# Kernel tuning notes

Measured on AMD Instinct MI355X. Metric: run time of the kernel, lower is better.

## Reference

```python
import jax, jax.numpy as jnp
import numpy as np

N_NODES = 50000
N_EDGES = 800000
IN_FEATS = 128
HIDDEN = 128
DNN_H = 256
N_CLASSES = 40


def setup_inputs() -> dict:
    key = jax.random.key(0)
    ks = jax.random.split(key, 12)
    features = jax.random.normal(ks[0], (N_NODES, IN_FEATS), dtype=jnp.float32)
    src = jax.random.randint(ks[1], (N_EDGES,), 0, N_NODES, dtype=jnp.int32)
    dst = jax.random.randint(ks[2], (N_EDGES,), 0, N_NODES, dtype=jnp.int32)
    def lin(k, fi, fo):
        s = 1.0 / np.sqrt(fi)
        return jax.random.uniform(k, (fi, fo), jnp.float32, -s, s)
    W1 = lin(ks[3], IN_FEATS, HIDDEN)
    b1 = jnp.zeros((HIDDEN,), jnp.float32)
    W2 = lin(ks[4], HIDDEN, HIDDEN)
    b2 = jnp.zeros((HIDDEN,), jnp.float32)
    Wd1 = lin(ks[5], HIDDEN, DNN_H)
    bd1 = jnp.zeros((DNN_H,), jnp.float32)
    Wd2 = lin(ks[6], DNN_H, N_CLASSES)
    bd2 = jnp.zeros((N_CLASSES,), jnp.float32)
    return {"features": features, "src": src, "dst": dst,
            "W1": W1, "b1": b1, "W2": W2, "b2": b2,
            "Wd1": Wd1, "bd1": bd1, "Wd2": Wd2, "bd2": bd2}


def _graph_conv(x, src, dst, W, b):
    # dgl GraphConv, norm='both': D_out^{-1/2} -> sum-aggregate -> D_in^{-1/2} -> linear -> relu
    ones = jnp.ones((src.shape[0],), x.dtype)
    deg_out = jax.ops.segment_sum(ones, src, num_segments=N_NODES)
    deg_in = jax.ops.segment_sum(ones, dst, num_segments=N_NODES)
    inv_sqrt_out = jax.lax.rsqrt(jnp.maximum(deg_out, 1.0))  # clamp zero-degree to 1 like dgl
    inv_sqrt_in = jax.lax.rsqrt(jnp.maximum(deg_in, 1.0))
    x = x * inv_sqrt_out[:, None]
    h = jax.ops.segment_sum(x[src], dst, num_segments=N_NODES)  # [N, d] sparse SpMM
    h = h * inv_sqrt_in[:, None]
    return jax.nn.relu(h @ W + b)


def reference(features, src, dst, W1, b1, W2, b2, Wd1, bd1, Wd2, bd2):
    h = _graph_conv(features, src, dst, W1, b1)   # dropout = identity (eval)
    h = _graph_conv(h, src, dst, W2, b2)
    # DNN: Linear -> LeakyReLU(0.01) -> (dropout identity), x2
    h = jax.nn.leaky_relu(h @ Wd1 + bd1, negative_slope=0.01)
    h = jax.nn.leaky_relu(h @ Wd2 + bd2, negative_slope=0.01)
    return h
```

## Files before the change

### kernel.cpp

```cpp
#include <hip/hip_runtime.h>


#define SCAN_B 256

typedef __attribute__((ext_vector_type(8))) short short8v;
typedef __attribute__((ext_vector_type(4))) float f32x4;

__global__ void k_degree_rank(const int* __restrict__ src, const int* __restrict__ dst,
                              int* __restrict__ deg_out, int* __restrict__ deg_in,
                              int* __restrict__ rank, int E) {
    int i = blockIdx.x * blockDim.x + threadIdx.x;
    if (i < E) {
        atomicAdd(&deg_out[src[i]], 1);
        rank[i] = atomicAdd(&deg_in[dst[i]], 1);
    }
}

__global__ void k_scanA(const int* __restrict__ deg_in, int* __restrict__ incl,
                        int* __restrict__ bsum, int N) {
    __shared__ int s[SCAN_B];
    int t = threadIdx.x, i = blockIdx.x * SCAN_B + t;
    int v = (i < N) ? deg_in[i] : 0;
    s[t] = v; __syncthreads();
    for (int o = 1; o < SCAN_B; o <<= 1) {
        int x = (t >= o) ? s[t - o] : 0;
        __syncthreads();
        s[t] += x;
        __syncthreads();
    }
    if (i < N) incl[i] = s[t];
    if (t == SCAN_B - 1) bsum[blockIdx.x] = s[t];
}

__global__ void k_scanB(int* __restrict__ bsum, int NB) {
    __shared__ int s[SCAN_B];
    int t = threadIdx.x;
    int v = (t < NB) ? bsum[t] : 0;
    s[t] = v; __syncthreads();
    for (int o = 1; o < SCAN_B; o <<= 1) {
        int x = (t >= o) ? s[t - o] : 0;
        __syncthreads();
        s[t] += x;
        __syncthreads();
    }
    if (t < NB) bsum[t] = s[t] - v;
}

__global__ void k_scanC(const int* __restrict__ deg_in, const int* __restrict__ deg_out,
                        int* __restrict__ row_ptr, const int* __restrict__ bsum,
                        float* __restrict__ inv_in, float* __restrict__ inv_out,
                        int N, int E) {
    int t = threadIdx.x, i = blockIdx.x * SCAN_B + t;
    if (i < N) {
        int di = deg_in[i];
        row_ptr[i] = row_ptr[i] - di + bsum[blockIdx.x];
        inv_in[i]  = rsqrtf(fmaxf((float)di, 1.0f));
        inv_out[i] = rsqrtf(fmaxf((float)deg_out[i], 1.0f));
    }
    if (i == 0) row_ptr[N] = E;
}

__global__ void k_scatter2(const int* __restrict__ src, const int* __restrict__ dst,
                           const int* __restrict__ row_ptr, const int* __restrict__ rank,
                           int* __restrict__ edge_src, int E) {
    int i = blockIdx.x * blockDim.x + threadIdx.x;
    if (i < E) {
        edge_src[row_ptr[dst[i]] + rank[i]] = src[i];
    }
}

__global__ void k_gather(const float* __restrict__ X, const int* __restrict__ edge_src,
                         const int* __restrict__ row_ptr, const float* __restrict__ inv_out,
                         const float* __restrict__ inv_in, float* __restrict__ Y, int N) {
    int lane = threadIdx.x & 31;
    int row = blockIdx.x * 8 + (threadIdx.x >> 5);
    if (row >= N) return;
    int rs = row_ptr[row], re = row_ptr[row + 1];
    float4 acc = {0.f, 0.f, 0.f, 0.f};
    for (int e = rs; e < re; ++e) {
        int s = edge_src[e];
        float sc = inv_out[s];
        float4 xv = *reinterpret_cast<const float4*>(&X[(size_t)s * 128 + lane * 4]);
        acc.x += xv.x * sc; acc.y += xv.y * sc; acc.z += xv.z * sc; acc.w += xv.w * sc;
    }
    float si = inv_in[row];
    float4 o = {acc.x * si, acc.y * si, acc.z * si, acc.w * si};
    *reinterpret_cast<float4*>(&Y[(size_t)row * 128 + lane * 4]) = o;
}

__device__ inline unsigned short bf16_rne(float f) {
    unsigned int u = __float_as_uint(f);
    u += 0x7fffu + ((u >> 16) & 1u);
    return (unsigned short)(u >> 16);
}

__device__ inline void split1(float a, unsigned short& h, unsigned short& l) {
    unsigned short hh = bf16_rne(a);
    float hf = __uint_as_float((unsigned int)hh << 16);
    l = bf16_rne(a - hf);
    h = hh;
}

template<int K, int N, int ACT>
__global__ __launch_bounds__(256) void k_gemm_mfma(const float* __restrict__ A,
                                                   const float* __restrict__ W,
                                                   const float* __restrict__ bias,
                                                   float* __restrict__ C, int M) {
    __shared__ unsigned short Bh[64 * K], Bl[64 * K];
    __shared__ unsigned short Ah[128 * 32], Al[128 * 32];

    int t = threadIdx.x;
    int m0 = blockIdx.x * 128;
    int cb = blockIdx.y * 64;

    {
        int c = t & 63;
        int kb = (t >> 6) * (K / 4);
        bool cok = (N % 64 == 0) || (cb + c < N);
        for (int j = 0; j < K / 4; ++j) {
            int k = kb + j;
            float v = cok ? W[(size_t)k * N + cb + c] : 0.f;
            unsigned short hi, lo; split1(v, hi, lo);
            int byte = (c * 2 * K + 2 * k) ^ ((c & 7) << 4);
            Bh[byte >> 1] = hi;
            Bl[byte >> 1] = lo;
        }
    }

    f32x4 acc[4][2];
    #pragma unroll
    for (int i = 0; i < 4; ++i)
        #pragma unroll
        for (int j = 0; j < 2; ++j)
            acc[i][j] = (f32x4){0.f, 0.f, 0.f, 0.f};

    int lane = t & 63;
    int wave = t >> 6;
    int wm = wave >> 1, wn = wave & 1;
    int lr = lane & 15, lg = lane >> 4;

    for (int kt = 0; kt < K / 32; ++kt) {
        __syncthreads();
        #pragma unroll
        for (int i = 0; i < 4; ++i) {
            int g = i * 256 + t;
            int r = g >> 3;
            int kq = (g & 7) * 4;
            int gr = m0 + r;
            float4 v = {0.f, 0.f, 0.f, 0.f};
            if (gr < M) v = *reinterpret_cast<const float4*>(&A[(size_t)gr * K + kt * 32 + kq]);
            ushort4 h4, l4;
            split1(v.x, h4.x, l4.x);
            split1(v.y, h4.y, l4.y);
            split1(v.z, h4.z, l4.z);
            split1(v.w, h4.w, l4.w);
            int byte = (r * 64 + 2 * kq) ^ ((r & 7) << 4);
            *reinterpret_cast<ushort4*>(&Ah[byte >> 1]) = h4;
            *reinterpret_cast<ushort4*>(&Al[byte >> 1]) = l4;
        }
        __syncthreads();

        short8v bhf[2], blf[2];
        #pragma unroll
        for (int nf = 0; nf < 2; ++nf) {
            int c = wn * 32 + nf * 16 + lr;
            int byte = (c * 2 * K + 2 * (kt * 32 + lg * 8)) ^ ((c & 7) << 4);
            bhf[nf] = *reinterpret_cast<const short8v*>(&Bh[byte >> 1]);
            blf[nf] = *reinterpret_cast<const short8v*>(&Bl[byte >> 1]);
        }
        #pragma unroll
        for (int mf = 0; mf < 4; ++mf) {
            int r = wm * 64 + mf * 16 + lr;
            int byte = (r * 64 + 2 * (lg * 8)) ^ ((r & 7) << 4);
            short8v ahf = *reinterpret_cast<const short8v*>(&Ah[byte >> 1]);
            short8v alf = *reinterpret_cast<const short8v*>(&Al[byte >> 1]);
            #pragma unroll
            for (int nf = 0; nf < 2; ++nf) {
                acc[mf][nf] = __builtin_amdgcn_mfma_f32_16x16x32_bf16(ahf, bhf[nf], acc[mf][nf], 0, 0, 0);
                acc[mf][nf] = __builtin_amdgcn_mfma_f32_16x16x32_bf16(ahf, blf[nf], acc[mf][nf], 0, 0, 0);
                acc[mf][nf] = __builtin_amdgcn_mfma_f32_16x16x32_bf16(alf, bhf[nf], acc[mf][nf], 0, 0, 0);
            }
        }
    }

    #pragma unroll
    for (int mf = 0; mf < 4; ++mf) {
        #pragma unroll
        for (int nf = 0; nf < 2; ++nf) {
            int col = cb + wn * 32 + nf * 16 + lr;
            if ((N % 64 != 0) && col >= N) continue;
            float bv = bias[col];
            #pragma unroll
            for (int rg = 0; rg < 4; ++rg) {
                int row = m0 + wm * 64 + mf * 16 + lg * 4 + rg;
                if (row < M) {
                    float v = acc[mf][nf][rg] + bv;
                    if (ACT == 0) v = fmaxf(v, 0.f);
                    else v = (v > 0.f) ? v : 0.01f * v;
                    C[(size_t)row * N + col] = v;
                }
            }
        }
    }
}

extern "C" void kernel_launch(void* const* d_in, const int* in_sizes, int n_in,
                              void* d_out, int out_size, void* d_ws, size_t ws_size,
                              hipStream_t stream) {
    const float* feat = (const float*)d_in[0];
    const int*   src  = (const int*)d_in[1];
    const int*   dst  = (const int*)d_in[2];
    const float* W1   = (const float*)d_in[3];
    const float* b1   = (const float*)d_in[4];
    const float* W2   = (const float*)d_in[5];
    const float* b2   = (const float*)d_in[6];
    const float* Wd1  = (const float*)d_in[7];
    const float* bd1  = (const float*)d_in[8];
    const float* Wd2  = (const float*)d_in[9];
    const float* bd2  = (const float*)d_in[10];
    float* out = (float*)d_out;

    const int N = in_sizes[0] / 128;
    const int E = in_sizes[1];

    char* ws = (char*)d_ws;
    size_t off = 0;
    auto alloc = [&](size_t bytes) -> void* {
        void* p = ws + off;
        off += (bytes + 255) & ~(size_t)255;
        return p;
    };
    int* deg_out  = (int*)alloc((size_t)N * 4);
    int* deg_in   = (int*)alloc((size_t)N * 4);
    int* row_ptr  = (int*)alloc((size_t)(N + 1) * 4);
    int* bsum     = (int*)alloc(SCAN_B * 4);
    int* rank     = (int*)alloc((size_t)E * 4);
    int* edge_src = (int*)alloc((size_t)E * 4);
    float* inv_out = (float*)alloc((size_t)N * 4);
    float* inv_in  = (float*)alloc((size_t)N * 4);
    float* agg = (float*)alloc((size_t)N * 128 * 4);
    float* h   = (float*)alloc((size_t)N * 128 * 4);
    float* hd  = (float*)alloc((size_t)N * 256 * 4);

    size_t zspan = (char*)deg_in + (size_t)N * 4 - (char*)deg_out;
    hipMemsetAsync(deg_out, 0, zspan, stream);

    int gE = (E + 255) / 256;
    int gN = (N + SCAN_B - 1) / SCAN_B;
    k_degree_rank<<<gE, 256, 0, stream>>>(src, dst, deg_out, deg_in, rank, E);
    k_scanA<<<gN, SCAN_B, 0, stream>>>(deg_in, row_ptr, bsum, N);
    k_scanB<<<1, SCAN_B, 0, stream>>>(bsum, gN);
    k_scanC<<<gN, SCAN_B, 0, stream>>>(deg_in, deg_out, row_ptr, bsum, inv_in, inv_out, N, E);
    k_scatter2<<<gE, 256, 0, stream>>>(src, dst, row_ptr, rank, edge_src, E);

    int gG = (N + 7) / 8;
    int gMM = (N + 127) / 128;

    k_gather<<<gG, 256, 0, stream>>>(feat, edge_src, row_ptr, inv_out, inv_in, agg, N);
    k_gemm_mfma<128, 128, 0><<<dim3(gMM, 2), 256, 0, stream>>>(agg, W1, b1, h, N);
    k_gather<<<gG, 256, 0, stream>>>(h, edge_src, row_ptr, inv_out, inv_in, agg, N);
    k_gemm_mfma<128, 128, 0><<<dim3(gMM, 2), 256, 0, stream>>>(agg, W2, b2, h, N);
    k_gemm_mfma<128, 256, 1><<<dim3(gMM, 4), 256, 0, stream>>>(h, Wd1, bd1, hd, N);
    k_gemm_mfma<256, 40, 1><<<dim3(gMM, 1), 256, 0, stream>>>(hd, Wd2, bd2, out, N);
}
```

Measured before the change: 379.1 us.

## Fuse degree counting into first GEMM, reorder GEMM before aggregation, pack edge weights

The first graph-conv layer now runs its linear transform before aggregation, which is valid because aggregation is linear. Bias and ReLU move into the gather kernel's epilogue. The degree/rank atomics are folded into the first GEMM launch, which removes a separate kernel. The scatter writes (src, inv_out[src]) pairs so the gather avoids a dependent lookup per edge, and the gather loop is unrolled by four to keep more row loads in flight. The cost is twice the memory for the edge array, and atomics contending inside GEMM blocks.

```diff
diff --git a/kernel.cpp b/kernel.cpp
--- a/kernel.cpp
+++ b/kernel.cpp
@@ -5,16 +5,6 @@
 
 typedef __attribute__((ext_vector_type(8))) short short8v;
 typedef __attribute__((ext_vector_type(4))) float f32x4;
-
-__global__ void k_degree_rank(const int* __restrict__ src, const int* __restrict__ dst,
-                              int* __restrict__ deg_out, int* __restrict__ deg_in,
-                              int* __restrict__ rank, int E) {
-    int i = blockIdx.x * blockDim.x + threadIdx.x;
-    if (i < E) {
-        atomicAdd(&deg_out[src[i]], 1);
-        rank[i] = atomicAdd(&deg_in[dst[i]], 1);
-    }
-}
 
 __global__ void k_scanA(const int* __restrict__ deg_in, int* __restrict__ incl,
                         int* __restrict__ bsum, int N) {
@@ -60,31 +50,54 @@
     if (i == 0) row_ptr[N] = E;
 }
 
-__global__ void k_scatter2(const int* __restrict__ src, const int* __restrict__ dst,
+__global__ void k_scatter3(const int* __restrict__ src, const int* __restrict__ dst,
                            const int* __restrict__ row_ptr, const int* __restrict__ rank,
-                           int* __restrict__ edge_src, int E) {
+                           const float* __restrict__ inv_out,
+                           int2* __restrict__ edges, int E) {
     int i = blockIdx.x * blockDim.x + threadIdx.x;
     if (i < E) {
-        edge_src[row_ptr[dst[i]] + rank[i]] = src[i];
-    }
-}
-
-__global__ void k_gather(const float* __restrict__ X, const int* __restrict__ edge_src,
-                         const int* __restrict__ row_ptr, const float* __restrict__ inv_out,
-                         const float* __restrict__ inv_in, float* __restrict__ Y, int N) {
+        int s = src[i];
+        int2 p;
+        p.x = s;
+        p.y = __float_as_int(inv_out[s]);
+        edges[row_ptr[dst[i]] + rank[i]] = p;
+    }
+}
+
+__global__ void k_gather2(const float* __restrict__ X, const int2* __restrict__ edges,
+                          const int* __restrict__ row_ptr, const float* __restrict__ inv_in,
+                          const float* __restrict__ bias, float* __restrict__ Y, int N) {
     int lane = threadIdx.x & 31;
     int row = blockIdx.x * 8 + (threadIdx.x >> 5);
     if (row >= N) return;
     int rs = row_ptr[row], re = row_ptr[row + 1];
     float4 acc = {0.f, 0.f, 0.f, 0.f};
-    for (int e = rs; e < re; ++e) {
-        int s = edge_src[e];
-        float sc = inv_out[s];
-        float4 xv = *reinterpret_cast<const float4*>(&X[(size_t)s * 128 + lane * 4]);
-        acc.x += xv.x * sc; acc.y += xv.y * sc; acc.z += xv.z * sc; acc.w += xv.w * sc;
-    }
+    int e = rs;
+    #define LDROW(s) (*reinterpret_cast<const float4*>(&X[(size_t)(s) * 128 + lane * 4]))
+    for (; e + 4 <= re; e += 4) {
+        int2 p0 = edges[e], p1 = edges[e + 1], p2 = edges[e + 2], p3 = edges[e + 3];
+        float4 x0 = LDROW(p0.x), x1 = LDROW(p1.x), x2 = LDROW(p2.x), x3 = LDROW(p3.x);
+        float c0 = __int_as_float(p0.y), c1 = __int_as_float(p1.y);
+        float c2 = __int_as_float(p2.y), c3 = __int_as_float(p3.y);
+        acc.x += c0 * x0.x + c1 * x1.x + c2 * x2.x + c3 * x3.x;
+        acc.y += c0 * x0.y + c1 * x1.y + c2 * x2.y + c3 * x3.y;
+        acc.z += c0 * x0.z + c1 * x1.z + c2 * x2.z + c3 * x3.z;
+        acc.w += c0 * x0.w + c1 * x1.w + c2 * x2.w + c3 * x3.w;
+    }
+    for (; e < re; ++e) {
+        int2 p = edges[e];
+        float c = __int_as_float(p.y);
+        float4 xv = LDROW(p.x);
+        acc.x += c * xv.x; acc.y += c * xv.y; acc.z += c * xv.z; acc.w += c * xv.w;
+    }
+    #undef LDROW
     float si = inv_in[row];
-    float4 o = {acc.x * si, acc.y * si, acc.z * si, acc.w * si};
+    float4 b4 = *reinterpret_cast<const float4*>(&bias[lane * 4]);
+    float4 o;
+    o.x = fmaxf(fmaf(acc.x, si, b4.x), 0.f);
+    o.y = fmaxf(fmaf(acc.y, si, b4.y), 0.f);
+    o.z = fmaxf(fmaf(acc.z, si, b4.z), 0.f);
+    o.w = fmaxf(fmaf(acc.w, si, b4.w), 0.f);
     *reinterpret_cast<float4*>(&Y[(size_t)row * 128 + lane * 4]) = o;
 }
 
@@ -101,15 +114,31 @@
     h = hh;
 }
 
-template<int K, int N, int ACT>
+template<int K, int N, int ACT, bool DEG>
 __global__ __launch_bounds__(256) void k_gemm_mfma(const float* __restrict__ A,
                                                    const float* __restrict__ W,
                                                    const float* __restrict__ bias,
-                                                   float* __restrict__ C, int M) {
+                                                   float* __restrict__ C, int M,
+                                                   const int* __restrict__ src,
+                                                   const int* __restrict__ dst,
+                                                   int* __restrict__ deg_out,
+                                                   int* __restrict__ deg_in,
+                                                   int* __restrict__ rank, int E, int epb) {
     __shared__ unsigned short Bh[64 * K], Bl[64 * K];
     __shared__ unsigned short Ah[128 * 32], Al[128 * 32];
 
     int t = threadIdx.x;
+
+    if (DEG) {
+        int bid = blockIdx.y * gridDim.x + blockIdx.x;
+        int base = bid * epb;
+        int end = min(E, base + epb);
+        for (int i = base + t; i < end; i += 256) {
+            atomicAdd(&deg_out[src[i]], 1);
+            rank[i] = atomicAdd(&deg_in[dst[i]], 1);
+        }
+    }
+
     int m0 = blockIdx.x * 128;
     int cb = blockIdx.y * 64;
 
@@ -189,14 +218,14 @@
         for (int nf = 0; nf < 2; ++nf) {
             int col = cb + wn * 32 + nf * 16 + lr;
             if ((N % 64 != 0) && col >= N) continue;
-            float bv = bias[col];
+            float bv = (ACT < 2) ? bias[col] : 0.f;
             #pragma unroll
             for (int rg = 0; rg < 4; ++rg) {
                 int row = m0 + wm * 64 + mf * 16 + lg * 4 + rg;
                 if (row < M) {
-                    float v = acc[mf][nf][rg] + bv;
-                    if (ACT == 0) v = fmaxf(v, 0.f);
-                    else v = (v > 0.f) ? v : 0.01f * v;
+                    float v = acc[mf][nf][rg];
+                    if (ACT == 0) v = fmaxf(v + bv, 0.f);
+                    else if (ACT == 1) { v += bv; v = (v > 0.f) ? v : 0.01f * v; }
                     C[(size_t)row * N + col] = v;
                 }
             }
@@ -235,31 +264,37 @@
     int* row_ptr  = (int*)alloc((size_t)(N + 1) * 4);
     int* bsum     = (int*)alloc(SCAN_B * 4);
     int* rank     = (int*)alloc((size_t)E * 4);
-    int* edge_src = (int*)alloc((size_t)E * 4);
+    int2* edges   = (int2*)alloc((size_t)E * 8);
     float* inv_out = (float*)alloc((size_t)N * 4);
     float* inv_in  = (float*)alloc((size_t)N * 4);
-    float* agg = (float*)alloc((size_t)N * 128 * 4);
-    float* h   = (float*)alloc((size_t)N * 128 * 4);
-    float* hd  = (float*)alloc((size_t)N * 256 * 4);
+    float* bufA = (float*)alloc((size_t)N * 128 * 4);
+    float* bufB = (float*)alloc((size_t)N * 128 * 4);
+    float* hd   = (float*)alloc((size_t)N * 256 * 4);
 
     size_t zspan = (char*)deg_in + (size_t)N * 4 - (char*)deg_out;
     hipMemsetAsync(deg_out, 0, zspan, stream);
 
     int gE = (E + 255) / 256;
     int gN = (N + SCAN_B - 1) / SCAN_B;
-    k_degree_rank<<<gE, 256, 0, stream>>>(src, dst, deg_out, deg_in, rank, E);
+    int gG = (N + 7) / 8;
+    int gMM = (N + 127) / 128;
+
+    int fusedBlocks = gMM * 2;
+    int epb = (E + fusedBlocks - 1) / fusedBlocks;
+    k_gemm_mfma<128, 128, 2, true><<<dim3(gMM, 2), 256, 0, stream>>>(
+        feat, W1, nullptr, bufA, N, src, dst, deg_out, deg_in, rank, E, epb);
+
     k_scanA<<<gN, SCAN_B, 0, stream>>>(deg_in, row_ptr, bsum, N);
     k_scanB<<<1, SCAN_B, 0, stream>>>(bsum, gN);
     k_scanC<<<gN, SCAN_B, 0, stream>>>(deg_in, deg_out, row_ptr, bsum, inv_in, inv_out, N, E);
-    k_scatter2<<<gE, 256, 0, stream>>>(src, dst, row_ptr, rank, edge_src, E);
-
-    int gG = (N + 7) / 8;
-    int gMM = (N + 127) / 128;
-
-    k_gather<<<gG, 256, 0, stream>>>(feat, edge_src, row_ptr, inv_out, inv_in, agg, N);
-    k_gemm_mfma<128, 128, 0><<<dim3(gMM, 2), 256, 0, stream>>>(agg, W1, b1, h, N);
-    k_gather<<<gG, 256, 0, stream>>>(h, edge_src, row_ptr, inv_out, inv_in, agg, N);
-    k_gemm_mfma<128, 128, 0><<<dim3(gMM, 2), 256, 0, stream>>>(agg, W2, b2, h, N);
-    k_gemm_mfma<128, 256, 1><<<dim3(gMM, 4), 256, 0, stream>>>(h, Wd1, bd1, hd, N);
-    k_gemm_mfma<256, 40, 1><<<dim3(gMM, 1), 256, 0, stream>>>(hd, Wd2, bd2, out, N);
-}
+    k_scatter3<<<gE, 256, 0, stream>>>(src, dst, row_ptr, rank, inv_out, edges, E);
+
+    k_gather2<<<gG, 256, 0, stream>>>(bufA, edges, row_ptr, inv_in, b1, bufB, N);
+    k_gemm_mfma<128, 128, 2, false><<<dim3(gMM, 2), 256, 0, stream>>>(
+        bufB, W2, nullptr, bufA, N, nullptr, nullptr, nullptr, nullptr, nullptr, 0, 0);
+    k_gather2<<<gG, 256, 0, stream>>>(bufA, edges, row_ptr, inv_in, b2, bufB, N);
+    k_gemm_mfma<128, 256, 1, false><<<dim3(gMM, 4), 256, 0, stream>>>(
+        bufB, Wd1, bd1, hd, N, nullptr, nullptr, nullptr, nullptr, nullptr, 0, 0);
+    k_gemm_mfma<256, 40, 1, false><<<dim3(gMM, 1), 256, 0, stream>>>(
+        hd, Wd2, bd2, out, N, nullptr, nullptr, nullptr, nullptr, nullptr, 0, 0);
+}
```

Measured after the change: 348.5 us. 8.1% less time.
